# Optimization experiments

Hardware: AMD Instinct MI355X
Metric: run time of the kernel (lower is better)

Reference implementation:

```python
import jax, jax.numpy as jnp
import numpy as np

INPUT_DIM = 6
HIDDEN = 256
NUM_CLASSES = 8
B = 16
V = 32768


def setup_inputs() -> dict:
    key = jax.random.key(0)
    ks = jax.random.split(key, 8)
    x = jax.random.normal(ks[0], (B, INPUT_DIM, V), dtype=jnp.float32)
    obj_idx = jax.random.randint(ks[1], (B,), 0, NUM_CLASSES)
    # Stacked per-class expert weights (Conv1d kernel_size=1 == pointwise linear)
    s1 = 1.0 / np.sqrt(INPUT_DIM)
    s2 = 1.0 / np.sqrt(HIDDEN)
    w1 = jax.random.uniform(ks[2], (NUM_CLASSES, HIDDEN, INPUT_DIM), jnp.float32, -s1, s1)
    b1 = jax.random.uniform(ks[3], (NUM_CLASSES, HIDDEN), jnp.float32, -s1, s1)
    w2 = jax.random.uniform(ks[4], (NUM_CLASSES, HIDDEN, HIDDEN), jnp.float32, -s2, s2)
    b2 = jax.random.uniform(ks[5], (NUM_CLASSES, HIDDEN), jnp.float32, -s2, s2)
    w3 = jax.random.uniform(ks[6], (NUM_CLASSES, 1, HIDDEN), jnp.float32, -s2, s2)
    b3 = jax.random.uniform(ks[7], (NUM_CLASSES, 1), jnp.float32, -s2, s2)
    return {"x": x, "obj_idx": obj_idx, "w1": w1, "b1": b1,
            "w2": w2, "b2": b2, "w3": w3, "b3": b3}


def reference(x, obj_idx, w1, b1, w2, b2, w3, b3):
    # Gather each sample's expert weights, then run the fused 3-layer pointwise
    # MLP over all B*V positions in one batched einsum per layer (no Python
    # loop over samples, unlike the original torch code).
    # x: [B, 6, V] -> out: [B, 1, V]
    h = jax.nn.relu(jnp.einsum('boi,biv->bov', w1[obj_idx], x) + b1[obj_idx][:, :, None])
    h = jax.nn.relu(jnp.einsum('boi,biv->bov', w2[obj_idx], h) + b2[obj_idx][:, :, None])
    out = jnp.einsum('boi,biv->bov', w3[obj_idx], h) + b3[obj_idx][:, :, None]
    return out
```

## Files before the change

### kernel.cpp

```cpp
#include <hip/hip_runtime.h>
#include <hip/hip_bf16.h>

typedef __bf16 bf16x8 __attribute__((ext_vector_type(8)));
typedef __bf16 bf16x4 __attribute__((ext_vector_type(4)));
typedef float  f32x4  __attribute__((ext_vector_type(4)));

#define V_TOTAL 32768
#define NT      512
#define NV      32
#define NBLK    256

#define W2_LDS  131072
#define H1_LDS  32768
#define LDS_TOT (W2_LDS + H1_LDS)

#define GLOAD_LDS16(g, l) __builtin_amdgcn_global_load_lds( \
    (const __attribute__((address_space(1))) void*)(g),     \
    (__attribute__((address_space(3))) void*)(l), 16, 0, 0)

__global__ void w2_to_bf16(const float* __restrict__ w2, __bf16* __restrict__ w2b) {
    int i = blockIdx.x * 256 + threadIdx.x;
    w2b[i] = (__bf16)w2[i];
}

__global__ __launch_bounds__(NT) void fused_mlp(
    const float* __restrict__ x,  const int* __restrict__ obj,
    const float* __restrict__ w1, const float* __restrict__ b1,
    const float* __restrict__ b2, const float* __restrict__ w3,
    const float* __restrict__ b3, const __bf16* __restrict__ w2b,
    float* __restrict__ out)
{
    extern __shared__ __align__(16) char smem[];
    char*  w2s = smem;
    char*  h1t = smem + W2_LDS;
    float* red = (float*)h1t;

    const int t    = threadIdx.x;
    const int lane = t & 63;
    const int wv   = t >> 6;
    const int llo  = lane & 15;
    const int lhi  = lane >> 4;
    const int b    = blockIdx.x >> 4;
    const int g    = blockIdx.x & 15;
    const int e    = __builtin_amdgcn_readfirstlane(obj[b]);
    const __bf16* w2e = w2b + (size_t)e * 65536;

    #pragma unroll
    for (int it = 0; it < 16; ++it) {
        int c    = it * NT + wv * 64 + lane;
        int kt   = c >> 10;
        int mt16 = (c >> 6) & 15;
        int ko   = (c >> 4) & 3;
        int row  = c & 15;
        GLOAD_LDS16(w2e + (mt16 * 16 + row) * 256 + kt * 32 + ko * 8,
                    w2s + (it * NT + wv * 64) * 16);
    }

    const float* w1e = w1 + e * 1536;
    bf16x8 aa1[2];
    f32x4  b1f[2], bv[2], wf[2];
    #pragma unroll
    for (int mt2 = 0; mt2 < 2; ++mt2) {
        const int m0 = (2 * wv + mt2) * 16;
        bf16x8 v = {};
        if (lhi == 0)
            #pragma unroll
            for (int j = 0; j < 6; ++j) v[j] = (__bf16)w1e[(m0 + llo) * 6 + j];
        aa1[mt2] = v;
        b1f[mt2] = *(const f32x4*)(b1 + e * 256 + m0 + lhi * 4);
        bv[mt2]  = *(const f32x4*)(b2 + e * 256 + m0 + lhi * 4);
        wf[mt2]  = *(const f32x4*)(w3 + e * 256 + m0 + lhi * 4);
    }
    const float b3e = b3[e];
    const float* xe = x + (size_t)b * 6 * V_TOTAL;

    bf16x8 xf[4];
    #pragma unroll
    for (int pt = 0; pt < 4; ++pt) {
        bf16x8 v = {};
        #pragma unroll
        for (int i = 0; i < 6; ++i)
            v[i] = (__bf16)xe[i * V_TOTAL + g * (NV * 64) + pt * 16 + llo];
        xf[pt] = v;
    }

    for (int iv = 0; iv < NV; ++iv) {
        const int v0 = (g * NV + iv) * 64;

        #pragma unroll
        for (int mt2 = 0; mt2 < 2; ++mt2) {
            const int o = (2 * wv + mt2) * 2 + (lhi >> 1);
            char* wbase = h1t + (o >> 2) * 4096 + (o & 3) * 256
                              + llo * 16 + (lhi & 1) * 8;
            #pragma unroll
            for (int pt = 0; pt < 4; ++pt) {
                f32x4 h = __builtin_amdgcn_mfma_f32_16x16x32_bf16(
                    aa1[mt2], xf[pt], b1f[mt2], 0, 0, 0);
                bf16x4 pk;
                #pragma unroll
                for (int r = 0; r < 4; ++r) pk[r] = (__bf16)fmaxf(h[r], 0.f);
                *(bf16x4*)(wbase + pt * 1024) = pk;
            }
        }
        if (iv + 1 < NV)
            #pragma unroll
            for (int pt = 0; pt < 4; ++pt) {
                bf16x8 v = {};
                #pragma unroll
                for (int i = 0; i < 6; ++i)
                    v[i] = (__bf16)xe[i * V_TOTAL + v0 + 64 + pt * 16 + llo];
                xf[pt] = v;
            }
        __syncthreads();

        f32x4 acc[2][4];
        #pragma unroll
        for (int mt = 0; mt < 2; ++mt)
            #pragma unroll
            for (int nt = 0; nt < 4; ++nt) acc[mt][nt] = bv[mt];
        const char* abase = w2s + wv * 2048 + lane * 16;
        const char* bbase = h1t + lane * 16;
        __builtin_amdgcn_s_setprio(1);
        #pragma unroll
        for (int kt = 0; kt < 8; ++kt) {
            bf16x8 bb[4];
            #pragma unroll
            for (int nt = 0; nt < 4; ++nt)
                bb[nt] = *(const bf16x8*)(bbase + kt * 4096 + nt * 1024);
            #pragma unroll
            for (int mt = 0; mt < 2; ++mt) {
                const bf16x8 aw = *(const bf16x8*)(abase + kt * 16384 + mt * 1024);
                #pragma unroll
                for (int nt = 0; nt < 4; ++nt)
                    acc[mt][nt] = __builtin_amdgcn_mfma_f32_16x16x32_bf16(
                        aw, bb[nt], acc[mt][nt], 0, 0, 0);
            }
        }
        __builtin_amdgcn_s_setprio(0);

        float p[4];
        #pragma unroll
        for (int nt = 0; nt < 4; ++nt) {
            float s = 0.f;
            #pragma unroll
            for (int mt = 0; mt < 2; ++mt)
                #pragma unroll
                for (int j = 0; j < 4; ++j)
                    s = fmaf(wf[mt][j], fmaxf(acc[mt][nt][j], 0.f), s);
            s += __shfl_xor(s, 16, 64);
            s += __shfl_xor(s, 32, 64);
            p[nt] = s;
        }
        __syncthreads();
        if (lane < 16)
            #pragma unroll
            for (int nt = 0; nt < 4; ++nt)
                red[wv * 64 + nt * 16 + lane] = p[nt];
        __syncthreads();
        if (t < 64) {
            float s = b3e;
            #pragma unroll
            for (int w8 = 0; w8 < 8; ++w8) s += red[w8 * 64 + t];
            out[(size_t)b * V_TOTAL + v0 + t] = s;
        }
        __syncthreads();
    }
}

extern "C" void kernel_launch(void* const* d_in, const int* in_sizes, int n_in,
                              void* d_out, int out_size, void* d_ws, size_t ws_size,
                              hipStream_t stream) {
    const float* x   = (const float*)d_in[0];
    const int*   obj = (const int*)d_in[1];
    const float* w1  = (const float*)d_in[2];
    const float* b1  = (const float*)d_in[3];
    const float* w2  = (const float*)d_in[4];
    const float* b2  = (const float*)d_in[5];
    const float* w3  = (const float*)d_in[6];
    const float* b3  = (const float*)d_in[7];
    float*  out = (float*)d_out;
    __bf16* w2b = (__bf16*)d_ws;

    (void)hipFuncSetAttribute((const void*)fused_mlp,
                              hipFuncAttributeMaxDynamicSharedMemorySize, LDS_TOT);

    w2_to_bf16<<<2048, 256, 0, stream>>>(w2, w2b);
    fused_mlp<<<NBLK, NT, LDS_TOT, stream>>>(x, obj, w1, b1, b2, w3, b3, w2b, out);
}
```

Before: 89.55 us.

## Double-buffer reduction LDS, hold last W2 k-tile in registers, pre-swizzle W2

The reduction scratch moves to its own double-buffered LDS region, so two of the four block barriers per iteration can be dropped. The final k-tile of W2 is held in registers instead of LDS, which shrinks the W2 LDS footprint. The bf16 conversion kernel now writes W2 in the MFMA tile order, so the async global-to-LDS copy becomes a contiguous stream. The cost is extra VGPRs for the held tile and more index arithmetic in the conversion kernel.

```diff
diff --git a/kernel.cpp b/kernel.cpp
--- a/kernel.cpp
+++ b/kernel.cpp
@@ -10,9 +10,10 @@
 #define NV      32
 #define NBLK    256
 
-#define W2_LDS  131072
+#define W2_LDS  114688
 #define H1_LDS  32768
-#define LDS_TOT (W2_LDS + H1_LDS)
+#define RED_LDS 4096
+#define LDS_TOT (W2_LDS + H1_LDS + RED_LDS)
 
 #define GLOAD_LDS16(g, l) __builtin_amdgcn_global_load_lds( \
     (const __attribute__((address_space(1))) void*)(g),     \
@@ -20,7 +21,9 @@
 
 __global__ void w2_to_bf16(const float* __restrict__ w2, __bf16* __restrict__ w2b) {
     int i = blockIdx.x * 256 + threadIdx.x;
-    w2b[i] = (__bf16)w2[i];
+    int e = i >> 16, q = i & 65535, c = q >> 3, j = q & 7;
+    int kt = c >> 10, mt16 = (c >> 6) & 15, ko = (c >> 4) & 3, row = c & 15;
+    w2b[i] = (__bf16)w2[e * 65536 + (mt16 * 16 + row) * 256 + kt * 32 + ko * 8 + j];
 }
 
 __global__ __launch_bounds__(NT) void fused_mlp(
@@ -33,7 +36,7 @@
     extern __shared__ __align__(16) char smem[];
     char*  w2s = smem;
     char*  h1t = smem + W2_LDS;
-    float* red = (float*)h1t;
+    float* red = (float*)(smem + W2_LDS + H1_LDS);
 
     const int t    = threadIdx.x;
     const int lane = t & 63;
@@ -43,17 +46,19 @@
     const int b    = blockIdx.x >> 4;
     const int g    = blockIdx.x & 15;
     const int e    = __builtin_amdgcn_readfirstlane(obj[b]);
-    const __bf16* w2e = w2b + (size_t)e * 65536;
-
-    #pragma unroll
-    for (int it = 0; it < 16; ++it) {
-        int c    = it * NT + wv * 64 + lane;
-        int kt   = c >> 10;
-        int mt16 = (c >> 6) & 15;
-        int ko   = (c >> 4) & 3;
-        int row  = c & 15;
-        GLOAD_LDS16(w2e + (mt16 * 16 + row) * 256 + kt * 32 + ko * 8,
-                    w2s + (it * NT + wv * 64) * 16);
+    const __bf16* w2sw = w2b + (size_t)e * 65536;
+
+    #pragma unroll
+    for (int it = 0; it < 14; ++it) {
+        int c0 = it * NT + wv * 64;
+        GLOAD_LDS16(w2sw + c0 * 8 + lane * 8, w2s + c0 * 16);
+    }
+
+    bf16x8 aa7[2];
+    #pragma unroll
+    for (int mt = 0; mt < 2; ++mt) {
+        int c = 7168 + (2 * wv + mt) * 64 + lane;
+        aa7[mt] = *(const bf16x8*)(w2sw + c * 8);
     }
 
     const float* w1e = w1 + e * 1536;
@@ -122,7 +127,7 @@
         const char* bbase = h1t + lane * 16;
         __builtin_amdgcn_s_setprio(1);
         #pragma unroll
-        for (int kt = 0; kt < 8; ++kt) {
+        for (int kt = 0; kt < 7; ++kt) {
             bf16x8 bb[4];
             #pragma unroll
             for (int nt = 0; nt < 4; ++nt)
@@ -135,6 +140,18 @@
                     acc[mt][nt] = __builtin_amdgcn_mfma_f32_16x16x32_bf16(
                         aw, bb[nt], acc[mt][nt], 0, 0, 0);
             }
+        }
+        {
+            bf16x8 bb[4];
+            #pragma unroll
+            for (int nt = 0; nt < 4; ++nt)
+                bb[nt] = *(const bf16x8*)(bbase + 7 * 4096 + nt * 1024);
+            #pragma unroll
+            for (int mt = 0; mt < 2; ++mt)
+                #pragma unroll
+                for (int nt = 0; nt < 4; ++nt)
+                    acc[mt][nt] = __builtin_amdgcn_mfma_f32_16x16x32_bf16(
+                        aa7[mt], bb[nt], acc[mt][nt], 0, 0, 0);
         }
         __builtin_amdgcn_s_setprio(0);
 
@@ -151,19 +168,18 @@
             s += __shfl_xor(s, 32, 64);
             p[nt] = s;
         }
-        __syncthreads();
+        float* rp = red + (iv & 1) * 512;
         if (lane < 16)
             #pragma unroll
             for (int nt = 0; nt < 4; ++nt)
-                red[wv * 64 + nt * 16 + lane] = p[nt];
+                rp[wv * 64 + nt * 16 + lane] = p[nt];
         __syncthreads();
         if (t < 64) {
             float s = b3e;
             #pragma unroll
-            for (int w8 = 0; w8 < 8; ++w8) s += red[w8 * 64 + t];
+            for (int w8 = 0; w8 < 8; ++w8) s += rp[w8 * 64 + t];
             out[(size_t)b * V_TOTAL + v0 + t] = s;
         }
-        __syncthreads();
     }
 }
 
```

After: 84.16 us. 1.06x faster.
